# Kernel tuning notes

Measured on AMD Instinct MI355X. Metric: run time of the kernel, lower is better.

## Reference

```python
import jax, jax.numpy as jnp
import numpy as np

D_MODEL = 1024
NUM_HEADS = 16
HEAD_DIM = D_MODEL // NUM_HEADS
R = 1.0
LAM = 0.1
CLIP_MIN = -15.0
CLIP_MAX = 15.0
EPS = 1e-9


def setup_inputs() -> dict:
    key = jax.random.key(0)
    k1, k2 = jax.random.split(key, 2)
    B, S = 2, 2048
    x = jax.random.normal(k1, (B, S, D_MODEL), dtype=jnp.float32)
    # NonNeg-constrained dense kernel -> nonnegative uniform init (small scale)
    W = jax.random.uniform(k2, (D_MODEL, D_MODEL), dtype=jnp.float32) * 0.02
    b = jnp.zeros((D_MODEL,), dtype=jnp.float32)
    d_q = jnp.ones((D_MODEL,), dtype=jnp.float32)
    d_k = jnp.ones((D_MODEL,), dtype=jnp.float32)
    d_v = jnp.ones((D_MODEL,), dtype=jnp.float32)
    return {"x": x, "W": W, "b": b, "d_q": d_q, "d_k": d_k, "d_v": d_v}


def _convex_r_softmax(z):
    z = jnp.clip(z, CLIP_MIN, CLIP_MAX)
    numerator = jax.nn.relu(jnp.exp(z - R) + LAM * z)
    denominator = jnp.sum(numerator, axis=-1, keepdims=True) + EPS
    return numerator / denominator


def reference(x, W, b, d_q, d_k, d_v):
    B, S, _ = x.shape
    x_proj = x @ W + b                      # [B, S, D]
    # diagonal scaling then split heads: [B, H, S, Dh]
    def heads(t):
        return t.reshape(B, S, NUM_HEADS, HEAD_DIM).transpose(0, 2, 1, 3)
    Q = heads(x_proj * d_q)
    K = heads(x_proj * d_k)
    V = heads(x_proj * d_v)
    scores = jnp.einsum('bhqd,bhkd->bhqk', Q, K)   # [B, H, S, S]
    attn = _convex_r_softmax(scores)
    out = jnp.einsum('bhqk,bhkd->bhqd', attn, V)   # [B, H, S, Dh]
    return out.transpose(0, 2, 1, 3).reshape(B, S, D_MODEL)
```

## Files before the change

### kernel.cpp

```cpp
#include <hip/hip_runtime.h>
#include <math.h>

#define D_MODEL   1024
#define NUM_HEADS 16
#define HEAD_DIM  64
#define S_LEN     2048
#define BATCH     2
#define M_TOT     (BATCH * S_LEN)

typedef __attribute__((ext_vector_type(8))) short short8;
typedef __attribute__((ext_vector_type(4))) short short4v;
typedef __attribute__((ext_vector_type(4))) float f32x4;

static __device__ __forceinline__ short f2bf(float f) {
    unsigned u = __builtin_bit_cast(unsigned, f);
    unsigned r = (u + 0x7FFFu + ((u >> 16) & 1u)) >> 16;
    return (short)r;
}

typedef __attribute__((address_space(3))) void lds_v;
typedef const __attribute__((address_space(1))) void glb_v;
static __device__ __forceinline__ void gll16(const void* g, void* l) {
    __builtin_amdgcn_global_load_lds((glb_v*)g, (lds_v*)l, 16, 0, 0);
}


__global__ __launch_bounds__(256) void cvt_x_kernel(
    const float* __restrict__ x, short* __restrict__ xb)
{
    int i = (blockIdx.x * 256 + threadIdx.x) * 8;
    float4 a = *(const float4*)(x + i);
    float4 b = *(const float4*)(x + i + 4);
    short8 o;
    o[0] = f2bf(a.x); o[1] = f2bf(a.y); o[2] = f2bf(a.z); o[3] = f2bf(a.w);
    o[4] = f2bf(b.x); o[5] = f2bf(b.y); o[6] = f2bf(b.z); o[7] = f2bf(b.w);
    *(short8*)(xb + i) = o;
}

__global__ __launch_bounds__(256) void cvt_w_kernel(
    const float* __restrict__ W, short* __restrict__ wt)
{
    __shared__ short T[64][72];
    const int tid = threadIdx.x;
    const int k0 = blockIdx.y * 64, n0 = blockIdx.x * 64;
    const int r = tid >> 4, c4 = (tid & 15) * 4;
    #pragma unroll
    for (int i = 0; i < 4; i++) {
        int kr = r + 16 * i;
        float4 v = *(const float4*)(W + (size_t)(k0 + kr) * D_MODEL + n0 + c4);
        short4v s;
        s[0] = f2bf(v.x); s[1] = f2bf(v.y); s[2] = f2bf(v.z); s[3] = f2bf(v.w);
        *(short4v*)&T[kr][c4] = s;
    }
    __syncthreads();
    const int n = tid >> 2, kb = (tid & 3) * 16;
    short tmp[16];
    #pragma unroll
    for (int j = 0; j < 16; j++) tmp[j] = T[kb + j][n];
    *(short8*)(wt + (size_t)(n0 + n) * D_MODEL + k0 + kb)     = *(short8*)&tmp[0];
    *(short8*)(wt + (size_t)(n0 + n) * D_MODEL + k0 + kb + 8) = *(short8*)&tmp[8];
}

__global__ __launch_bounds__(256) void gemm_qkv_kernel(
    const short* __restrict__ xb, const short* __restrict__ wt,
    const float* __restrict__ bias, const float* __restrict__ dq,
    const float* __restrict__ dk, const float* __restrict__ dv,
    short* __restrict__ Q, short* __restrict__ K, short* __restrict__ Vt)
{
    __shared__ __attribute__((aligned(16))) short lds[12288];

    const int tid  = threadIdx.x;
    const int w    = tid >> 6, l = tid & 63;
    const int quad = l >> 4,  c = l & 15;
    const int cx   = c & 7;
    const int n0 = blockIdx.x * 128, m0 = blockIdx.y * 64;
    const int wm = (w & 1) * 32, wn = (w >> 1) * 64;
    short* As = lds;
    short* Bs = lds + 4096;

    const int srow  = l >> 3;
    const int sslot = (l & 7) ^ srow;

    f32x4 acc[2][4];
    #pragma unroll
    for (int mi = 0; mi < 2; mi++)
        #pragma unroll
        for (int ni = 0; ni < 4; ni++) acc[mi][ni] = (f32x4){0.f, 0.f, 0.f, 0.f};

    for (int k0 = 0; k0 < D_MODEL; k0 += 64) {
        __syncthreads();
        #pragma unroll
        for (int i = 0; i < 2; i++) {
            int rbase = 16 * w + 8 * i;
            gll16(xb + (size_t)(m0 + rbase + srow) * D_MODEL + k0 + sslot * 8,
                  As + rbase * 64);
        }
        #pragma unroll
        for (int i = 0; i < 4; i++) {
            int rbase = 32 * w + 8 * i;
            gll16(wt + (size_t)(n0 + rbase + srow) * D_MODEL + k0 + sslot * 8,
                  Bs + rbase * 64);
        }
        __syncthreads();
        #pragma unroll
        for (int kh = 0; kh < 2; kh++) {
            const int sx = (kh * 4 + quad) ^ cx;
            short8 af[2], bf[4];
            #pragma unroll
            for (int mi = 0; mi < 2; mi++)
                af[mi] = *(const short8*)&As[(wm + 16 * mi + c) * 64 + sx * 8];
            #pragma unroll
            for (int ni = 0; ni < 4; ni++)
                bf[ni] = *(const short8*)&Bs[(wn + 16 * ni + c) * 64 + sx * 8];
            #pragma unroll
            for (int mi = 0; mi < 2; mi++)
                #pragma unroll
                for (int ni = 0; ni < 4; ni++)
                    acc[mi][ni] = __builtin_amdgcn_mfma_f32_16x16x32_bf16(
                        af[mi], bf[ni], acc[mi][ni], 0, 0, 0);
        }
    }

    __syncthreads();
    const int b      = m0 >> 11;
    const int s_base = m0 & 2047;
    const int h      = (n0 + wn) >> 6;

    float biasv[4], dqv[4], dkv[4], dvv[4];
    #pragma unroll
    for (int ni = 0; ni < 4; ni++) {
        int n_g = n0 + wn + 16 * ni + c;
        biasv[ni] = bias[n_g]; dqv[ni] = dq[n_g];
        dkv[ni] = dk[n_g];     dvv[ni] = dv[n_g];
    }

    short* E = lds;
    #pragma unroll
    for (int mi = 0; mi < 2; mi++) {
        #pragma unroll
        for (int ni = 0; ni < 4; ni++) {
            short4v vv;
            #pragma unroll
            for (int r = 0; r < 4; r++) {
                float xv = acc[mi][ni][r] + biasv[ni];
                int s = s_base + wm + 16 * mi + 4 * quad + r;
                size_t off = (((size_t)(b * NUM_HEADS + h) * S_LEN + s) << 6) + (16 * ni + c);
                Q[off] = f2bf(xv * dqv[ni]);
                K[off] = f2bf(xv * dkv[ni]);
                vv[r]  = f2bf(xv * dvv[ni]);
            }
            int n_l = wn + 16 * ni + c;
            int m_l = wm + 16 * mi + 4 * quad;
            *(short4v*)&E[n_l * 72 + m_l] = vv;
        }
    }
    __syncthreads();
    {
        const int n_l = tid >> 1, mh = (tid & 1) * 32;
        const int h2 = (n0 + n_l) >> 6;
        const int dh = n_l & 63;
        short* dst = Vt + ((size_t)(b * NUM_HEADS + h2) * HEAD_DIM + dh) * S_LEN + s_base;
        #pragma unroll
        for (int ch = 0; ch < 4; ch++) {
            short8 v = *(const short8*)&E[n_l * 72 + mh + ch * 8];
            *(short8*)(dst + mh + ch * 8) = v;
        }
    }
}

__global__ __launch_bounds__(256) void attn2_kernel(
    const short* __restrict__ Q, const short* __restrict__ K,
    const short* __restrict__ Vt, float* __restrict__ out)
{
    __shared__ __attribute__((aligned(16))) short lds[8192 + 4 * 32 * 88];

    const int tid  = threadIdx.x;
    const int w    = tid >> 6, l = tid & 63;
    const int quad = l >> 4,  c = l & 15;
    const int cx   = c & 7;
    const int q0 = blockIdx.x * 128;
    const int h  = blockIdx.y, b = blockIdx.z;
    const size_t bh = (size_t)(b * NUM_HEADS + h);
    const short* Qh  = Q  + bh * S_LEN * HEAD_DIM;
    const short* Kh  = K  + bh * S_LEN * HEAD_DIM;
    const short* Vth = Vt + bh * HEAD_DIM * S_LEN;

    short* Ks = lds;
    short* Vs = lds + 4096;
    short* Ps = lds + 8192 + w * (32 * 88);

    const int srow  = l >> 3;
    const int sslot = (l & 7) ^ srow;

    short8 qf0[2], qf1[2];
    {
        const short* qp0 = Qh + (size_t)(q0 + 32 * w + c) * 64 + quad * 8;
        const short* qp1 = qp0 + 16 * 64;
        qf0[0] = *(const short8*)(qp0);
        qf0[1] = *(const short8*)(qp0 + 32);
        qf1[0] = *(const short8*)(qp1);
        qf1[1] = *(const short8*)(qp1 + 32);
    }

    f32x4 o0[4], o1[4];
    #pragma unroll
    for (int i = 0; i < 4; i++) {
        o0[i] = (f32x4){0.f, 0.f, 0.f, 0.f};
        o1[i] = (f32x4){0.f, 0.f, 0.f, 0.f};
    }
    float dnm0 = 0.0f, dnm1 = 0.0f;

    for (int kt = 0; kt < S_LEN / 64; kt++) {
        const int k0 = kt * 64;
        __syncthreads();
        #pragma unroll
        for (int i = 0; i < 2; i++) {
            int rbase = 16 * w + 8 * i;
            int row = rbase + srow;
            gll16(Kh + (size_t)(k0 + row) * 64 + sslot * 8, Ks + rbase * 64);
            gll16(Vth + (size_t)row * S_LEN + k0 + sslot * 8, Vs + rbase * 64);
        }
        __syncthreads();

        f32x4 s0[4], s1[4];
        #pragma unroll
        for (int n = 0; n < 4; n++) {
            s0[n] = (f32x4){0.f, 0.f, 0.f, 0.f};
            s1[n] = (f32x4){0.f, 0.f, 0.f, 0.f};
        }
        #pragma unroll
        for (int hh = 0; hh < 2; hh++) {
            const int sx = (hh * 4 + quad) ^ cx;
            #pragma unroll
            for (int n = 0; n < 4; n++) {
                short8 kf = *(const short8*)&Ks[(16 * n + c) * 64 + sx * 8];
                s0[n] = __builtin_amdgcn_mfma_f32_16x16x32_bf16(kf, qf0[hh], s0[n], 0, 0, 0);
                s1[n] = __builtin_amdgcn_mfma_f32_16x16x32_bf16(kf, qf1[hh], s1[n], 0, 0, 0);
            }
        }

        #pragma unroll
        for (int n = 0; n < 4; n++) {
            float nm[4];
            #pragma unroll
            for (int r = 0; r < 4; r++) {
                float z = __builtin_amdgcn_fmed3f(s0[n][r], -15.0f, 15.0f);
                float e = __builtin_amdgcn_exp2f(
                    __builtin_fmaf(z, 1.4426950408889634f, -1.4426950408889634f));
                float num = fmaxf(__builtin_fmaf(z, 0.1f, e), 0.0f);
                dnm0 += num;
                nm[r] = num;
            }
            unsigned p0 = __builtin_amdgcn_perm(
                __builtin_bit_cast(unsigned, nm[1]) + 0x8000u,
                __builtin_bit_cast(unsigned, nm[0]) + 0x8000u, 0x07060302u);
            unsigned p1 = __builtin_amdgcn_perm(
                __builtin_bit_cast(unsigned, nm[3]) + 0x8000u,
                __builtin_bit_cast(unsigned, nm[2]) + 0x8000u, 0x07060302u);
            uint2 pr; pr.x = p0; pr.y = p1;
            *(uint2*)&Ps[c * 88 + 16 * n + 4 * quad] = pr;
        }
        #pragma unroll
        for (int n = 0; n < 4; n++) {
            float nm[4];
            #pragma unroll
            for (int r = 0; r < 4; r++) {
                float z = __builtin_amdgcn_fmed3f(s1[n][r], -15.0f, 15.0f);
                float e = __builtin_amdgcn_exp2f(
                    __builtin_fmaf(z, 1.4426950408889634f, -1.4426950408889634f));
                float num = fmaxf(__builtin_fmaf(z, 0.1f, e), 0.0f);
                dnm1 += num;
                nm[r] = num;
            }
            unsigned p0 = __builtin_amdgcn_perm(
                __builtin_bit_cast(unsigned, nm[1]) + 0x8000u,
                __builtin_bit_cast(unsigned, nm[0]) + 0x8000u, 0x07060302u);
            unsigned p1 = __builtin_amdgcn_perm(
                __builtin_bit_cast(unsigned, nm[3]) + 0x8000u,
                __builtin_bit_cast(unsigned, nm[2]) + 0x8000u, 0x07060302u);
            uint2 pr; pr.x = p0; pr.y = p1;
            *(uint2*)&Ps[(16 + c) * 88 + 16 * n + 4 * quad] = pr;
        }

        #pragma unroll
        for (int kh = 0; kh < 2; kh++) {
            short8 pf0 = *(const short8*)&Ps[c * 88 + 32 * kh + 8 * quad];
            short8 pf1 = *(const short8*)&Ps[(16 + c) * 88 + 32 * kh + 8 * quad];
            const int sx = (kh * 4 + quad) ^ cx;
            #pragma unroll
            for (int n2 = 0; n2 < 4; n2++) {
                short8 vf = *(const short8*)&Vs[(16 * n2 + c) * 64 + sx * 8];
                o0[n2] = __builtin_amdgcn_mfma_f32_16x16x32_bf16(pf0, vf, o0[n2], 0, 0, 0);
                o1[n2] = __builtin_amdgcn_mfma_f32_16x16x32_bf16(pf1, vf, o1[n2], 0, 0, 0);
            }
        }
    }

    dnm0 += __shfl_xor(dnm0, 16, 64);
    dnm0 += __shfl_xor(dnm0, 32, 64);
    dnm1 += __shfl_xor(dnm1, 16, 64);
    dnm1 += __shfl_xor(dnm1, 32, 64);

    #pragma unroll
    for (int r = 0; r < 4; r++) {
        float dr0 = __shfl(dnm0, quad * 4 + r, 64);
        float dr1 = __shfl(dnm1, quad * 4 + r, 64);
        float inv0 = 1.0f / (dr0 + 1e-9f);
        float inv1 = 1.0f / (dr1 + 1e-9f);
        int qrow0 = q0 + 32 * w + 4 * quad + r;
        float* op0 = out + ((size_t)(b * S_LEN + qrow0) << 10) + (h << 6) + c;
        float* op1 = op0 + (16 << 10);
        #pragma unroll
        for (int n2 = 0; n2 < 4; n2++) {
            op0[16 * n2] = o0[n2][r] * inv0;
            op1[16 * n2] = o1[n2][r] * inv1;
        }
    }
}

__global__ __launch_bounds__(256, 4) void gemm_xw_kernel(
    const float* __restrict__ x, const float* __restrict__ W,
    const float* __restrict__ bias, float* __restrict__ xp)
{
    __shared__ float Asf[64][36];
    __shared__ float Bsf[32][68];

    const int tid = threadIdx.x;
    const int tx  = tid & 15;
    const int ty  = tid >> 4;
    const int m0  = blockIdx.y * 64;
    const int n0  = blockIdx.x * 64;

    float acc[4][4];
    #pragma unroll
    for (int i = 0; i < 4; i++)
        #pragma unroll
        for (int j = 0; j < 4; j++) acc[i][j] = 0.0f;

    for (int k0 = 0; k0 < D_MODEL; k0 += 32) {
        #pragma unroll
        for (int i = 0; i < 2; i++) {
            int idx = tid + i * 256;
            int r = idx >> 3, c4 = idx & 7;
            *(float4*)(&Asf[r][c4 * 4]) =
                *(const float4*)(x + (size_t)(m0 + r) * D_MODEL + k0 + c4 * 4);
        }
        #pragma unroll
        for (int i = 0; i < 2; i++) {
            int idx = tid + i * 256;
            int r = idx >> 4, c4 = idx & 15;
            *(float4*)(&Bsf[r][c4 * 4]) =
                *(const float4*)(W + (size_t)(k0 + r) * D_MODEL + n0 + c4 * 4);
        }
        __syncthreads();
        #pragma unroll
        for (int k = 0; k < 32; k += 4) {
            float a[4][4];
            #pragma unroll
            for (int i = 0; i < 4; i++) {
                float4 t = *(const float4*)(&Asf[ty + 16 * i][k]);
                a[i][0] = t.x; a[i][1] = t.y; a[i][2] = t.z; a[i][3] = t.w;
            }
            #pragma unroll
            for (int kk = 0; kk < 4; kk++) {
                float4 bv = *(const float4*)(&Bsf[k + kk][tx * 4]);
                #pragma unroll
                for (int i = 0; i < 4; i++) {
                    acc[i][0] += a[i][kk] * bv.x;
                    acc[i][1] += a[i][kk] * bv.y;
                    acc[i][2] += a[i][kk] * bv.z;
                    acc[i][3] += a[i][kk] * bv.w;
                }
            }
        }
        __syncthreads();
    }
    float4 bv = *(const float4*)(bias + n0 + tx * 4);
    #pragma unroll
    for (int i = 0; i < 4; i++) {
        float4 r;
        r.x = acc[i][0] + bv.x; r.y = acc[i][1] + bv.y;
        r.z = acc[i][2] + bv.z; r.w = acc[i][3] + bv.w;
        *(float4*)(xp + (size_t)(m0 + ty + 16 * i) * D_MODEL + n0 + tx * 4) = r;
    }
}

__global__ __launch_bounds__(256, 4) void attn_fb_kernel(
    const float* __restrict__ xp, const float* __restrict__ dq,
    const float* __restrict__ dk, const float* __restrict__ dv,
    float* __restrict__ out)
{
    __shared__ __attribute__((aligned(16))) short lds[13824];

    const int tid  = threadIdx.x;
    const int wave = tid >> 6;
    const int l    = tid & 63;
    const int quad = l >> 4;
    const int c    = l & 15;
    const int q0   = blockIdx.x * 64;
    const int h    = blockIdx.y;
    const int bb   = blockIdx.z;
    const int col0 = h * HEAD_DIM;
    const float* base = xp + (size_t)bb * S_LEN * D_MODEL;

    short* Ks = lds;
    short* Vt = lds + 64 * 72;
    short* Ps = lds + 2 * 64 * 72 + wave * (16 * 72);

    short8 qf[2];
    {
        const int qrow = q0 + wave * 16 + c;
        const float* qp = base + (size_t)qrow * D_MODEL + col0 + quad * 8;
        const float* sp = dq + col0 + quad * 8;
        #pragma unroll
        for (int hh = 0; hh < 2; hh++) {
            float4 v0 = *(const float4*)(qp + 32 * hh);
            float4 v1 = *(const float4*)(qp + 32 * hh + 4);
            float4 s0 = *(const float4*)(sp + 32 * hh);
            float4 s1 = *(const float4*)(sp + 32 * hh + 4);
            qf[hh][0] = f2bf(v0.x * s0.x); qf[hh][1] = f2bf(v0.y * s0.y);
            qf[hh][2] = f2bf(v0.z * s0.z); qf[hh][3] = f2bf(v0.w * s0.w);
            qf[hh][4] = f2bf(v1.x * s1.x); qf[hh][5] = f2bf(v1.y * s1.y);
            qf[hh][6] = f2bf(v1.z * s1.z); qf[hh][7] = f2bf(v1.w * s1.w);
        }
    }

    const int sc4  = 4 * (tid & 15);
    const int srow = tid >> 4;
    const float4 ksc = *(const float4*)(dk + col0 + sc4);
    const int vd = tid & 63;
    const int vg = tid >> 6;
    const float vsc = dv[col0 + vd];

    f32x4 acc_o[4];
    #pragma unroll
    for (int i = 0; i < 4; i++) acc_o[i] = (f32x4){0.f, 0.f, 0.f, 0.f};
    float dnm = 0.0f;

    for (int kt = 0; kt < S_LEN / 64; kt++) {
        const int k0 = kt * 64;
        __syncthreads();

        #pragma unroll
        for (int i = 0; i < 4; i++) {
            int r = srow + 16 * i;
            float4 v = *(const float4*)(base + (size_t)(k0 + r) * D_MODEL + col0 + sc4);
            short4v s;
            s[0] = f2bf(v.x * ksc.x); s[1] = f2bf(v.y * ksc.y);
            s[2] = f2bf(v.z * ksc.z); s[3] = f2bf(v.w * ksc.w);
            *(short4v*)&Ks[r * 72 + sc4] = s;
        }
        #pragma unroll
        for (int p = 0; p < 4; p++) {
            int kb = 16 * p + 4 * vg;
            const float* vp = base + (size_t)(k0 + kb) * D_MODEL + col0 + vd;
            float a0 = vp[0 * D_MODEL], a1 = vp[1 * D_MODEL];
            float a2 = vp[2 * D_MODEL], a3 = vp[3 * D_MODEL];
            short4v s;
            s[0] = f2bf(a0 * vsc); s[1] = f2bf(a1 * vsc);
            s[2] = f2bf(a2 * vsc); s[3] = f2bf(a3 * vsc);
            *(short4v*)&Vt[vd * 72 + kb] = s;
        }
        __syncthreads();

        f32x4 sacc[4];
        #pragma unroll
        for (int n = 0; n < 4; n++) sacc[n] = (f32x4){0.f, 0.f, 0.f, 0.f};
        #pragma unroll
        for (int n = 0; n < 4; n++)
            #pragma unroll
            for (int hh = 0; hh < 2; hh++) {
                short8 kf = *(const short8*)&Ks[(16 * n + c) * 72 + 32 * hh + 8 * quad];
                sacc[n] = __builtin_amdgcn_mfma_f32_16x16x32_bf16(kf, qf[hh], sacc[n], 0, 0, 0);
            }

        #pragma unroll
        for (int n = 0; n < 4; n++) {
            short4v pp;
            #pragma unroll
            for (int r = 0; r < 4; r++) {
                float z = fminf(fmaxf(sacc[n][r], -15.0f), 15.0f);
                float e = __expf(z - 1.0f);
                float num = fmaxf(fmaf(z, 0.1f, e), 0.0f);
                dnm += num;
                pp[r] = f2bf(num);
            }
            *(short4v*)&Ps[c * 72 + 16 * n + 4 * quad] = pp;
        }

        #pragma unroll
        for (int kh = 0; kh < 2; kh++) {
            short8 pf = *(const short8*)&Ps[c * 72 + 32 * kh + 8 * quad];
            #pragma unroll
            for (int n2 = 0; n2 < 4; n2++) {
                short8 vf = *(const short8*)&Vt[(16 * n2 + c) * 72 + 32 * kh + 8 * quad];
                acc_o[n2] = __builtin_amdgcn_mfma_f32_16x16x32_bf16(pf, vf, acc_o[n2], 0, 0, 0);
            }
        }
    }

    dnm += __shfl_xor(dnm, 16, 64);
    dnm += __shfl_xor(dnm, 32, 64);

    #pragma unroll
    for (int r = 0; r < 4; r++) {
        float dr  = __shfl(dnm, quad * 4 + r, 64);
        float inv = 1.0f / (dr + 1e-9f);
        const int qrow = q0 + wave * 16 + quad * 4 + r;
        float* op = out + (size_t)(bb * S_LEN + qrow) * D_MODEL + col0 + c;
        #pragma unroll
        for (int n2 = 0; n2 < 4; n2++)
            op[16 * n2] = acc_o[n2][r] * inv;
    }
}

extern "C" void kernel_launch(void* const* d_in, const int* in_sizes, int n_in,
                              void* d_out, int out_size, void* d_ws, size_t ws_size,
                              hipStream_t stream) {
    const float* x  = (const float*)d_in[0];
    const float* W  = (const float*)d_in[1];
    const float* bias = (const float*)d_in[2];
    const float* dq = (const float*)d_in[3];
    const float* dk = (const float*)d_in[4];
    const float* dv = (const float*)d_in[5];
    float* out = (float*)d_out;

    const size_t XB_B = (size_t)M_TOT * D_MODEL * 2;
    const size_t WT_B = (size_t)D_MODEL * D_MODEL * 2;
    const size_t T_B  = (size_t)BATCH * NUM_HEADS * S_LEN * HEAD_DIM * 2;
    const size_t NEED = XB_B + WT_B + 3 * T_B;

    if (ws_size >= NEED) {
        char* p = (char*)d_ws;
        short* xb = (short*)p;             p += XB_B;
        short* wt = (short*)p;             p += WT_B;
        short* Qt = (short*)p;             p += T_B;
        short* Kt = (short*)p;             p += T_B;
        short* Vt = (short*)p;

        cvt_x_kernel<<<(M_TOT * D_MODEL) / 2048, 256, 0, stream>>>(x, xb);
        dim3 gw(D_MODEL / 64, D_MODEL / 64);
        cvt_w_kernel<<<gw, 256, 0, stream>>>(W, wt);
        dim3 gg(D_MODEL / 128, M_TOT / 64);
        gemm_qkv_kernel<<<gg, 256, 0, stream>>>(xb, wt, bias, dq, dk, dv, Qt, Kt, Vt);
        dim3 ga(S_LEN / 128, NUM_HEADS, BATCH);
        attn2_kernel<<<ga, 256, 0, stream>>>(Qt, Kt, Vt, out);
    } else {
        float* xp = (float*)d_ws;
        dim3 g1(D_MODEL / 64, M_TOT / 64);
        gemm_xw_kernel<<<g1, 256, 0, stream>>>(x, W, bias, xp);
        dim3 g2(S_LEN / 64, NUM_HEADS, BATCH);
        attn_fb_kernel<<<g2, 256, 0, stream>>>(xp, dq, dk, dv, out);
    }
}
```

Measured before the change: 167.4 us.

## Split attention over key range into two partial passes with combine kernel

Adds a split-K attention kernel that processes half the key sequence per block, doubling grid size from 512 to 1024 blocks, writing fp32 partial outputs and row sums, then a combine kernel that sums partials, normalizes and writes output. Also merges the x and W conversion kernels into one launch. The aim is better occupancy across the many CUs. The cost is extra global traffic for fp32 partials (about 64MB written and read) and an extra launch. The new path runs only if the workspace is large enough.

Measured after the change: 171.5 us. +2.5%, slower.

```diff
diff --git a/kernel.cpp b/kernel.cpp
--- a/kernel.cpp
+++ b/kernel.cpp
@@ -25,40 +25,41 @@
 }
 
 
-__global__ __launch_bounds__(256) void cvt_x_kernel(
-    const float* __restrict__ x, short* __restrict__ xb)
-{
-    int i = (blockIdx.x * 256 + threadIdx.x) * 8;
-    float4 a = *(const float4*)(x + i);
-    float4 b = *(const float4*)(x + i + 4);
-    short8 o;
-    o[0] = f2bf(a.x); o[1] = f2bf(a.y); o[2] = f2bf(a.z); o[3] = f2bf(a.w);
-    o[4] = f2bf(b.x); o[5] = f2bf(b.y); o[6] = f2bf(b.z); o[7] = f2bf(b.w);
-    *(short8*)(xb + i) = o;
-}
-
-__global__ __launch_bounds__(256) void cvt_w_kernel(
+__global__ __launch_bounds__(256) void cvt_xw_kernel(
+    const float* __restrict__ x, short* __restrict__ xb,
     const float* __restrict__ W, short* __restrict__ wt)
 {
     __shared__ short T[64][72];
-    const int tid = threadIdx.x;
-    const int k0 = blockIdx.y * 64, n0 = blockIdx.x * 64;
-    const int r = tid >> 4, c4 = (tid & 15) * 4;
-    #pragma unroll
-    for (int i = 0; i < 4; i++) {
-        int kr = r + 16 * i;
-        float4 v = *(const float4*)(W + (size_t)(k0 + kr) * D_MODEL + n0 + c4);
-        short4v s;
-        s[0] = f2bf(v.x); s[1] = f2bf(v.y); s[2] = f2bf(v.z); s[3] = f2bf(v.w);
-        *(short4v*)&T[kr][c4] = s;
-    }
-    __syncthreads();
-    const int n = tid >> 2, kb = (tid & 3) * 16;
-    short tmp[16];
-    #pragma unroll
-    for (int j = 0; j < 16; j++) tmp[j] = T[kb + j][n];
-    *(short8*)(wt + (size_t)(n0 + n) * D_MODEL + k0 + kb)     = *(short8*)&tmp[0];
-    *(short8*)(wt + (size_t)(n0 + n) * D_MODEL + k0 + kb + 8) = *(short8*)&tmp[8];
+    const int bx = blockIdx.x;
+    if (bx < 2048) {
+        int i = (bx * 256 + threadIdx.x) * 8;
+        float4 a = *(const float4*)(x + i);
+        float4 b = *(const float4*)(x + i + 4);
+        short8 o;
+        o[0] = f2bf(a.x); o[1] = f2bf(a.y); o[2] = f2bf(a.z); o[3] = f2bf(a.w);
+        o[4] = f2bf(b.x); o[5] = f2bf(b.y); o[6] = f2bf(b.z); o[7] = f2bf(b.w);
+        *(short8*)(xb + i) = o;
+    } else {
+        const int t = bx - 2048;
+        const int tid = threadIdx.x;
+        const int k0 = (t >> 4) * 64, n0 = (t & 15) * 64;
+        const int r = tid >> 4, c4 = (tid & 15) * 4;
+        #pragma unroll
+        for (int i = 0; i < 4; i++) {
+            int kr = r + 16 * i;
+            float4 v = *(const float4*)(W + (size_t)(k0 + kr) * D_MODEL + n0 + c4);
+            short4v s;
+            s[0] = f2bf(v.x); s[1] = f2bf(v.y); s[2] = f2bf(v.z); s[3] = f2bf(v.w);
+            *(short4v*)&T[kr][c4] = s;
+        }
+        __syncthreads();
+        const int n = tid >> 2, kb = (tid & 3) * 16;
+        short tmp[16];
+        #pragma unroll
+        for (int j = 0; j < 16; j++) tmp[j] = T[kb + j][n];
+        *(short8*)(wt + (size_t)(n0 + n) * D_MODEL + k0 + kb)     = *(short8*)&tmp[0];
+        *(short8*)(wt + (size_t)(n0 + n) * D_MODEL + k0 + kb + 8) = *(short8*)&tmp[8];
+    }
 }
 
 __global__ __launch_bounds__(256) void gemm_qkv_kernel(
@@ -166,6 +167,179 @@
             *(short8*)(dst + mh + ch * 8) = v;
         }
     }
+}
+
+__global__ __launch_bounds__(256) void attn_split_kernel(
+    const short* __restrict__ Q, const short* __restrict__ K,
+    const short* __restrict__ Vt, float* __restrict__ Opart,
+    float* __restrict__ dpart)
+{
+    __shared__ __attribute__((aligned(16))) short lds[8192 + 4 * 32 * 88];
+
+    const int tid  = threadIdx.x;
+    const int w    = tid >> 6, l = tid & 63;
+    const int quad = l >> 4,  c = l & 15;
+    const int cx   = c & 7;
+    const int qt    = blockIdx.x >> 1;
+    const int split = blockIdx.x & 1;
+    const int q0 = qt * 128;
+    const int h  = blockIdx.y, b = blockIdx.z;
+    const size_t bh = (size_t)(b * NUM_HEADS + h);
+    const short* Qh  = Q  + bh * S_LEN * HEAD_DIM;
+    const short* Kh  = K  + bh * S_LEN * HEAD_DIM;
+    const short* Vth = Vt + bh * HEAD_DIM * S_LEN;
+
+    short* Ks = lds;
+    short* Vs = lds + 4096;
+    short* Ps = lds + 8192 + w * (32 * 88);
+
+    const int srow  = l >> 3;
+    const int sslot = (l & 7) ^ srow;
+
+    short8 qf0[2], qf1[2];
+    {
+        const short* qp0 = Qh + (size_t)(q0 + 32 * w + c) * 64 + quad * 8;
+        const short* qp1 = qp0 + 16 * 64;
+        qf0[0] = *(const short8*)(qp0);
+        qf0[1] = *(const short8*)(qp0 + 32);
+        qf1[0] = *(const short8*)(qp1);
+        qf1[1] = *(const short8*)(qp1 + 32);
+    }
+
+    short8 ones;
+    #pragma unroll
+    for (int j = 0; j < 8; j++) ones[j] = (short)0x3F80;
+
+    f32x4 o0[4], o1[4], d0a, d1a;
+    #pragma unroll
+    for (int i = 0; i < 4; i++) {
+        o0[i] = (f32x4){0.f, 0.f, 0.f, 0.f};
+        o1[i] = (f32x4){0.f, 0.f, 0.f, 0.f};
+    }
+    d0a = (f32x4){0.f, 0.f, 0.f, 0.f};
+    d1a = (f32x4){0.f, 0.f, 0.f, 0.f};
+
+    const int kt_beg = split * (S_LEN / 128);
+    for (int kt = kt_beg; kt < kt_beg + S_LEN / 128; kt++) {
+        const int k0 = kt * 64;
+        __syncthreads();
+        #pragma unroll
+        for (int i = 0; i < 2; i++) {
+            int rbase = 16 * w + 8 * i;
+            int row = rbase + srow;
+            gll16(Kh + (size_t)(k0 + row) * 64 + sslot * 8, Ks + rbase * 64);
+            gll16(Vth + (size_t)row * S_LEN + k0 + sslot * 8, Vs + rbase * 64);
+        }
+        __syncthreads();
+
+        f32x4 s0[4], s1[4];
+        #pragma unroll
+        for (int n = 0; n < 4; n++) {
+            s0[n] = (f32x4){0.f, 0.f, 0.f, 0.f};
+            s1[n] = (f32x4){0.f, 0.f, 0.f, 0.f};
+        }
+        #pragma unroll
+        for (int hh = 0; hh < 2; hh++) {
+            const int sx = (hh * 4 + quad) ^ cx;
+            #pragma unroll
+            for (int n = 0; n < 4; n++) {
+                short8 kf = *(const short8*)&Ks[(16 * n + c) * 64 + sx * 8];
+                s0[n] = __builtin_amdgcn_mfma_f32_16x16x32_bf16(kf, qf0[hh], s0[n], 0, 0, 0);
+                s1[n] = __builtin_amdgcn_mfma_f32_16x16x32_bf16(kf, qf1[hh], s1[n], 0, 0, 0);
+            }
+        }
+
+        #pragma unroll
+        for (int n = 0; n < 4; n++) {
+            float nm[4];
+            #pragma unroll
+            for (int r = 0; r < 4; r++) {
+                float z = __builtin_amdgcn_fmed3f(s0[n][r], -15.0f, 15.0f);
+                float e = __builtin_amdgcn_exp2f(
+                    __builtin_fmaf(z, 1.4426950408889634f, -1.4426950408889634f));
+                nm[r] = fmaxf(__builtin_fmaf(z, 0.1f, e), 0.0f);
+            }
+            unsigned p0 = __builtin_amdgcn_perm(
+                __builtin_bit_cast(unsigned, nm[1]) + 0x8000u,
+                __builtin_bit_cast(unsigned, nm[0]) + 0x8000u, 0x07060302u);
+            unsigned p1 = __builtin_amdgcn_perm(
+                __builtin_bit_cast(unsigned, nm[3]) + 0x8000u,
+                __builtin_bit_cast(unsigned, nm[2]) + 0x8000u, 0x07060302u);
+            uint2 pr; pr.x = p0; pr.y = p1;
+            *(uint2*)&Ps[c * 88 + 16 * n + 4 * quad] = pr;
+        }
+        #pragma unroll
+        for (int n = 0; n < 4; n++) {
+            float nm[4];
+            #pragma unroll
+            for (int r = 0; r < 4; r++) {
+                float z = __builtin_amdgcn_fmed3f(s1[n][r], -15.0f, 15.0f);
+                float e = __builtin_amdgcn_exp2f(
+                    __builtin_fmaf(z, 1.4426950408889634f, -1.4426950408889634f));
+                nm[r] = fmaxf(__builtin_fmaf(z, 0.1f, e), 0.0f);
+            }
+            unsigned p0 = __builtin_amdgcn_perm(
+                __builtin_bit_cast(unsigned, nm[1]) + 0x8000u,
+                __builtin_bit_cast(unsigned, nm[0]) + 0x8000u, 0x07060302u);
+            unsigned p1 = __builtin_amdgcn_perm(
+                __builtin_bit_cast(unsigned, nm[3]) + 0x8000u,
+                __builtin_bit_cast(unsigned, nm[2]) + 0x8000u, 0x07060302u);
+            uint2 pr; pr.x = p0; pr.y = p1;
+            *(uint2*)&Ps[(16 + c) * 88 + 16 * n + 4 * quad] = pr;
+        }
+
+        #pragma unroll
+        for (int kh = 0; kh < 2; kh++) {
+            short8 pf0 = *(const short8*)&Ps[c * 88 + 32 * kh + 8 * quad];
+            short8 pf1 = *(const short8*)&Ps[(16 + c) * 88 + 32 * kh + 8 * quad];
+            const int sx = (kh * 4 + quad) ^ cx;
+            #pragma unroll
+            for (int n2 = 0; n2 < 4; n2++) {
+                short8 vf = *(const short8*)&Vs[(16 * n2 + c) * 64 + sx * 8];
+                o0[n2] = __builtin_amdgcn_mfma_f32_16x16x32_bf16(pf0, vf, o0[n2], 0, 0, 0);
+                o1[n2] = __builtin_amdgcn_mfma_f32_16x16x32_bf16(pf1, vf, o1[n2], 0, 0, 0);
+            }
+            d0a = __builtin_amdgcn_mfma_f32_16x16x32_bf16(pf0, ones, d0a, 0, 0, 0);
+            d1a = __builtin_amdgcn_mfma_f32_16x16x32_bf16(pf1, ones, d1a, 0, 0, 0);
+        }
+    }
+
+    float* Op = Opart + ((((size_t)split * BATCH + b) * NUM_HEADS + h) * 16 + qt) * (128 * 64);
+    float* dp = dpart + ((((size_t)split * BATCH + b) * NUM_HEADS + h) * 16 + qt) * 128;
+
+    #pragma unroll
+    for (int r = 0; r < 4; r++) {
+        int row0 = 32 * w + 4 * quad + r;
+        #pragma unroll
+        for (int n2 = 0; n2 < 4; n2++) {
+            Op[row0 * 64 + 16 * n2 + c]        = o0[n2][r];
+            Op[(row0 + 16) * 64 + 16 * n2 + c] = o1[n2][r];
+        }
+        if (c == 0) {
+            dp[row0]      = d0a[r];
+            dp[row0 + 16] = d1a[r];
+        }
+    }
+}
+
+__global__ __launch_bounds__(256) void combine_kernel(
+    const float* __restrict__ Opart, const float* __restrict__ dpart,
+    float* __restrict__ out)
+{
+    const int gid = blockIdx.x * 256 + threadIdx.x;
+    const int row = gid >> 4;
+    const int col = (gid & 15) * 4;
+    float d = dpart[row] + dpart[65536 + row] + 1e-9f;
+    float inv = 1.0f / d;
+    float4 a = *(const float4*)(Opart + (size_t)gid * 4);
+    float4 bb = *(const float4*)(Opart + 4194304 + (size_t)gid * 4);
+    const int b = row >> 15;
+    const int h = (row >> 11) & 15;
+    const int s = row & 2047;
+    float4 r;
+    r.x = (a.x + bb.x) * inv; r.y = (a.y + bb.y) * inv;
+    r.z = (a.z + bb.z) * inv; r.w = (a.w + bb.w) * inv;
+    *(float4*)(out + ((size_t)(b * S_LEN + s) << 10) + (h << 6) + col) = r;
 }
 
 __global__ __launch_bounds__(256) void attn2_kernel(
@@ -528,23 +702,33 @@
     const size_t XB_B = (size_t)M_TOT * D_MODEL * 2;
     const size_t WT_B = (size_t)D_MODEL * D_MODEL * 2;
     const size_t T_B  = (size_t)BATCH * NUM_HEADS * S_LEN * HEAD_DIM * 2;
-    const size_t NEED = XB_B + WT_B + 3 * T_B;
-
-    if (ws_size >= NEED) {
+    const size_t OP_B = (size_t)2 * 65536 * 64 * 4;
+    const size_t DP_B = (size_t)2 * 65536 * 4;
+    const size_t NEED1 = XB_B + WT_B + 3 * T_B;
+    const size_t NEED2 = NEED1 + OP_B + DP_B;
+
+    if (ws_size >= NEED1) {
         char* p = (char*)d_ws;
         short* xb = (short*)p;             p += XB_B;
         short* wt = (short*)p;             p += WT_B;
         short* Qt = (short*)p;             p += T_B;
         short* Kt = (short*)p;             p += T_B;
-        short* Vt = (short*)p;
-
-        cvt_x_kernel<<<(M_TOT * D_MODEL) / 2048, 256, 0, stream>>>(x, xb);
-        dim3 gw(D_MODEL / 64, D_MODEL / 64);
-        cvt_w_kernel<<<gw, 256, 0, stream>>>(W, wt);
+        short* Vt = (short*)p;             p += T_B;
+
+        cvt_xw_kernel<<<2048 + 256, 256, 0, stream>>>(x, xb, W, wt);
         dim3 gg(D_MODEL / 128, M_TOT / 64);
         gemm_qkv_kernel<<<gg, 256, 0, stream>>>(xb, wt, bias, dq, dk, dv, Qt, Kt, Vt);
-        dim3 ga(S_LEN / 128, NUM_HEADS, BATCH);
-        attn2_kernel<<<ga, 256, 0, stream>>>(Qt, Kt, Vt, out);
+
+        if (ws_size >= NEED2) {
+            float* Opart = (float*)p;      p += OP_B;
+            float* dpart = (float*)p;
+            dim3 ga(2 * S_LEN / 128, NUM_HEADS, BATCH);
+            attn_split_kernel<<<ga, 256, 0, stream>>>(Qt, Kt, Vt, Opart, dpart);
+            combine_kernel<<<4096, 256, 0, stream>>>(Opart, dpart, out);
+        } else {
+            dim3 ga(S_LEN / 128, NUM_HEADS, BATCH);
+            attn2_kernel<<<ga, 256, 0, stream>>>(Qt, Kt, Vt, out);
+        }
     } else {
         float* xp = (float*)d_ws;
         dim3 g1(D_MODEL / 64, M_TOT / 64);
```
